# Performance work log

Hardware: AMD Instinct MI355X
Metric: run time of the kernel (lower is better)

## Reference

```python
import jax, jax.numpy as jnp
import numpy as np

B, L, D = 4, 2048, 512


def setup_inputs() -> dict:
    key = jax.random.key(0)
    ks = jax.random.split(key, 12)
    f32 = jnp.float32
    mk = lambda k, s: jax.random.normal(k, s, dtype=f32)
    # xavier-uniform-ish init scale for the linear weights
    w_qkv_lim = np.sqrt(6.0 / (6 * D + 6 * D)).astype(np.float32)
    w_out_lim = np.sqrt(6.0 / (2 * D + 2 * D)).astype(np.float32)
    return {
        "q_real": mk(ks[0], (B, L, D)),
        "q_imag": mk(ks[1], (B, L, D)),
        "k_real": mk(ks[2], (B, L, D)),
        "k_imag": mk(ks[3], (B, L, D)),
        "v_real": mk(ks[4], (B, L, D)),
        "v_imag": mk(ks[5], (B, L, D)),
        "pad_mask": jax.random.randint(ks[6], (B, L), 0, 2).astype(jnp.bool_),
        "W_qkv": jax.random.uniform(ks[7], (6 * D, 6 * D), f32, -w_qkv_lim, w_qkv_lim),
        "b_qkv": jnp.zeros((6 * D,), f32),
        "W_out": jax.random.uniform(ks[8], (2 * D, 2 * D), f32, -w_out_lim, w_out_lim),
        "b_out": jnp.zeros((2 * D,), f32),
    }


def reference(q_real, q_imag, k_real, k_imag, v_real, v_imag, pad_mask,
              W_qkv, b_qkv, W_out, b_out):
    b, l, d = q_real.shape
    # fused QKV projection over concatenated real/imag streams: [B, L, 6D]
    x = jnp.concatenate([q_real, q_imag, k_real, k_imag, v_real, v_imag], axis=-1)
    qkv = x @ W_qkv.T + b_qkv                      # torch Linear: x @ W^T + b
    qkv = qkv.reshape(b, l, 6, d)
    q_r, k_r = qkv[:, :, 0], qkv[:, :, 2]
    v_r, v_i = qkv[:, :, 4], qkv[:, :, 5]
    scale = jnp.asarray(d, jnp.float32) ** -0.5
    scores = jnp.einsum('bqd,bkd->bqk', q_r, k_r) * scale   # [B, L, L]
    scores = jnp.where(pad_mask[:, None, :], -jnp.inf, scores)
    attn = jax.nn.softmax(scores, axis=-1)         # dropout omitted (eval mode)
    out_real = jnp.einsum('bqk,bkd->bqd', attn, v_r)
    out_imag = jnp.einsum('bqk,bkd->bqd', attn, v_i)
    out = jnp.concatenate([out_real, out_imag], axis=-1) @ W_out.T + b_out
    return out[..., :d], out[..., d:]
```

## Files before the change

### kernel.cpp

```cpp
#include <hip/hip_runtime.h>
#include <cstdint>
#include <cstddef>

typedef unsigned short ushort;
typedef __attribute__((ext_vector_type(8))) short short8;
typedef __attribute__((ext_vector_type(16))) float f32x16;

__device__ __forceinline__ float bf2f(ushort u) {
  union { unsigned u; float f; } c; c.u = ((unsigned)u) << 16; return c.f;
}
__device__ __forceinline__ ushort f2bf(float f) {
  union { float f; unsigned u; } c; c.f = f;
  unsigned u = c.u;
  return (ushort)((u + 0x7fffu + ((u >> 16) & 1u)) >> 16);
}

#define G2L(g, l) __builtin_amdgcn_global_load_lds( \
    (const __attribute__((address_space(1))) void*)(g), \
    (__attribute__((address_space(3))) void*)(l), 16, 0, 0)

struct MArgs {
  const ushort* A; int lda; long asz;
  const ushort* B; int ldb; long bsz;
  void* C; int ldc; long csz;
  int K;
  const float* bias;
  float* C2;
};

template<int MODE, int BN>
__launch_bounds__(512, 2)
__global__ void mfma_gemm(MArgs g) {
  constexpr int BM = 256;
  constexpr int WN = BN / 64;
  constexpr int WM = 8 / WN;
  constexpr int WMSZ = BM / WM;
  constexpr int MF = WMSZ / 32;
  constexpr int NBG = BN / 64;
  constexpr int LPS = 4 + NBG;

  __shared__ __attribute__((aligned(16))) ushort As[2][BM * 64];
  __shared__ __attribute__((aligned(16))) ushort Bs[2][BN * 64];

  const int tid = threadIdx.x;
  const int lane = tid & 63;
  const int wave = tid >> 6;
  const int z = blockIdx.z;

  int bx = blockIdx.x, by = blockIdx.y;
  {
    const int gx = gridDim.x;
    const int nwg = gx * gridDim.y;
    int wg = by * gx + bx;
    wg = (wg & 7) * (nwg >> 3) + (wg >> 3);
    bx = wg % gx; by = wg / gx;
  }
  const long m0 = (long)by * BM;
  const long n0 = (long)bx * BN;
  const ushort* Ab = g.A + (long)z * g.asz;
  const ushort* Bb = g.B + (long)z * g.bsz;

  const int srow = tid >> 3;
  const long skel = (long)((((tid & 7) - srow) & 7) * 8);
  const ushort* ga[4];
  const ushort* gb[NBG];
#pragma unroll
  for (int q = 0; q < 4; ++q) ga[q] = Ab + (m0 + q * 64 + srow) * (long)g.lda + skel;
#pragma unroll
  for (int q = 0; q < NBG; ++q) gb[q] = Bb + (n0 + q * 64 + srow) * (long)g.ldb + skel;

  const int l31 = lane & 31, hb = lane >> 5;
  const int wmi = wave / WN, wni = wave % WN;
  int aoff[MF], arot[MF];
#pragma unroll
  for (int mf = 0; mf < MF; ++mf) {
    const int r = wmi * WMSZ + mf * 32 + l31;
    aoff[mf] = r * 64;
    arot[mf] = (r + hb) & 7;
  }
  int boff[2], brot[2];
#pragma unroll
  for (int nf = 0; nf < 2; ++nf) {
    const int r = wni * 64 + nf * 32 + l31;
    boff[nf] = r * 64;
    brot[nf] = (r + hb) & 7;
  }

  f32x16 acc[MF][2];
#pragma unroll
  for (int mf = 0; mf < MF; ++mf)
#pragma unroll
    for (int nf = 0; nf < 2; ++nf)
#pragma unroll
      for (int r = 0; r < 16; ++r) acc[mf][nf][r] = 0.f;

  auto STAGEF = [&](int buf, int t) {
    const long ko = (long)t * 64;
#pragma unroll
    for (int q = 0; q < 4; ++q) G2L(ga[q] + ko, &As[buf][q * 4096 + tid * 8]);
#pragma unroll
    for (int q = 0; q < NBG; ++q) G2L(gb[q] + ko, &Bs[buf][q * 4096 + tid * 8]);
  };

  STAGEF(0, 0);
  STAGEF(1, 1);

  const int nt = g.K >> 6;
  int cur = 0;
  for (int t = 0; t < nt; ++t) {
    if (t + 1 < nt) asm volatile("s_waitcnt vmcnt(%0)" :: "n"(LPS) : "memory");
    else            asm volatile("s_waitcnt vmcnt(0)" ::: "memory");
    __builtin_amdgcn_s_barrier();
    asm volatile("" ::: "memory");

    const ushort* as = &As[cur][0];
    const ushort* bs = &Bs[cur][0];
    __builtin_amdgcn_s_setprio(1);
#pragma unroll
    for (int h = 0; h < 4; ++h) {
      short8 av[MF], bv[2];
#pragma unroll
      for (int mf = 0; mf < MF; ++mf)
        av[mf] = *(const short8*)(as + aoff[mf] + (((2 * h + arot[mf]) & 7) << 3));
#pragma unroll
      for (int nf = 0; nf < 2; ++nf)
        bv[nf] = *(const short8*)(bs + boff[nf] + (((2 * h + brot[nf]) & 7) << 3));
#pragma unroll
      for (int mf = 0; mf < MF; ++mf)
#pragma unroll
        for (int nf = 0; nf < 2; ++nf)
          acc[mf][nf] = __builtin_amdgcn_mfma_f32_32x32x16_bf16(av[mf], bv[nf], acc[mf][nf], 0, 0, 0);
    }
    __builtin_amdgcn_s_setprio(0);

    asm volatile("s_waitcnt lgkmcnt(0)" ::: "memory");
    __builtin_amdgcn_s_barrier();
    asm volatile("" ::: "memory");
    if (t + 2 < nt) STAGEF(cur, t + 2);
    cur ^= 1;
  }

  const int cc = l31;
  const int rbase = 4 * hb;
  ushort* Cu = (ushort*)g.C + (long)z * g.csz;
  float* Cf = (float*)g.C;
#pragma unroll
  for (int mf = 0; mf < MF; ++mf) {
#pragma unroll
    for (int nf = 0; nf < 2; ++nf) {
      const long col = n0 + wni * 64 + nf * 32 + cc;
      float bsv = 0.f;
      if (MODE == 0 || MODE == 3) bsv = g.bias[col];
#pragma unroll
      for (int r = 0; r < 16; ++r) {
        const long row = m0 + wmi * WMSZ + mf * 32 + (r & 3) + 8 * (r >> 2) + rbase;
        float v = acc[mf][nf][r] + bsv;
        if (MODE == 3) {
          float* dst = (col < 512) ? (Cf + row * 512 + col) : (g.C2 + row * 512 + (col - 512));
          *dst = v;
        } else {
          Cu[row * (long)g.ldc + col] = f2bf(v);
        }
      }
    }
  }
}

__global__ void cvt_x6(const float* x0, const float* x1, const float* x2,
                       const float* x3, const float* x4, const float* x5, ushort* X) {
  const long m = blockIdx.y;
  const int c4 = (blockIdx.x * 256 + threadIdx.x) * 4;
  const int p = c4 >> 9, d = c4 & 511;
  const float* xp;
  switch (p) {
    case 0: xp = x0; break; case 1: xp = x1; break; case 2: xp = x2; break;
    case 3: xp = x3; break; case 4: xp = x4; break; default: xp = x5; break;
  }
  float4 v = *(const float4*)(xp + m * 512 + d);
  ushort4 o; o.x = f2bf(v.x); o.y = f2bf(v.y); o.z = f2bf(v.z); o.w = f2bf(v.w);
  *(ushort4*)(X + m * 3072 + c4) = o;
}

__device__ __forceinline__ int chunk_map(int c) { return (c == 0) ? 0 : (c == 1) ? 2 : (c == 2) ? 4 : 5; }

__global__ void cvt_w4(const float* W, ushort* Wq4) {
  const long r = blockIdx.y;
  const int c4 = (blockIdx.x * 256 + threadIdx.x) * 4;
  const long wr = (long)chunk_map((int)(r >> 9)) * 512 + (r & 511);
  float4 v = *(const float4*)(W + wr * 3072 + c4);
  ushort4 o; o.x = f2bf(v.x); o.y = f2bf(v.y); o.z = f2bf(v.z); o.w = f2bf(v.w);
  *(ushort4*)(Wq4 + r * 3072 + c4) = o;
}

__global__ void cvt_wout(const float* W, ushort* Wo) {
  const long r = blockIdx.y;
  const int c4 = threadIdx.x * 4;
  float4 v = *(const float4*)(W + r * 1024 + c4);
  ushort4 o; o.x = f2bf(v.x); o.y = f2bf(v.y); o.z = f2bf(v.z); o.w = f2bf(v.w);
  *(ushort4*)(Wo + r * 1024 + c4) = o;
}

__global__ void mk_bias4(const float* bqkv, float* b4) {
  const int n = blockIdx.x * 256 + threadIdx.x;
  b4[n] = bqkv[chunk_map(n >> 9) * 512 + (n & 511)];
}

__global__ void transpose_v(const ushort* QKV, ushort* Vt) {
  __shared__ ushort t[64][65];
  const int tid = threadIdx.x;
  const int k0 = blockIdx.x * 64, n0 = blockIdx.y * 64, b = blockIdx.z;
  const ushort* src = QKV + (long)b * 2048 * 2048 + 1024;
#pragma unroll
  for (int i = 0; i < 16; ++i) {
    int idx = i * 256 + tid; int r = idx >> 6, c = idx & 63;
    t[r][c] = src[(long)(k0 + r) * 2048 + (n0 + c)];
  }
  __syncthreads();
  ushort* dst = Vt + (long)b * 1024 * 2048;
#pragma unroll
  for (int i = 0; i < 16; ++i) {
    int idx = i * 256 + tid; int r = idx >> 6, c = idx & 63;
    dst[(long)(n0 + r) * 2048 + (k0 + c)] = t[c][r];
  }
}

__launch_bounds__(256)
__global__ void softmax_rows(ushort* S, const int* mask) {
  const int lane = threadIdx.x & 63;
  const int wave = threadIdx.x >> 6;
  const long row = (long)blockIdx.x * 4 + wave;
  const int* m = mask + (row >> 11) * 2048 + lane * 32;
  ushort* s = S + row * 2048 + lane * 32;
  const float scale = 0.04419417382415922f;

  short8 raw[4];
#pragma unroll
  for (int i = 0; i < 4; ++i) raw[i] = *(const short8*)(s + i * 8);
  int4 mi[8];
#pragma unroll
  for (int i = 0; i < 8; ++i) mi[i] = *(const int4*)(m + i * 4);

  float v[32];
  int mk[32];
#pragma unroll
  for (int i = 0; i < 8; ++i) {
    mk[i * 4 + 0] = mi[i].x; mk[i * 4 + 1] = mi[i].y;
    mk[i * 4 + 2] = mi[i].z; mk[i * 4 + 3] = mi[i].w;
  }
#pragma unroll
  for (int i = 0; i < 32; ++i) v[i] = bf2f((ushort)raw[i >> 3][i & 7]) * scale;

  float mx = -INFINITY;
#pragma unroll
  for (int i = 0; i < 32; ++i) if (!mk[i]) mx = fmaxf(mx, v[i]);
#pragma unroll
  for (int off = 32; off; off >>= 1) mx = fmaxf(mx, __shfl_xor(mx, off));

  float sum = 0.f;
#pragma unroll
  for (int i = 0; i < 32; ++i) {
    float e = mk[i] ? 0.f : __expf(v[i] - mx);
    v[i] = e;
    sum += e;
  }
#pragma unroll
  for (int off = 32; off; off >>= 1) sum += __shfl_xor(sum, off);

  float r = 1.f / sum;
  short8 out[4];
#pragma unroll
  for (int i = 0; i < 32; ++i) out[i >> 3][i & 7] = (short)f2bf(v[i] * r);
#pragma unroll
  for (int i = 0; i < 4; ++i) *(short8*)(s + i * 8) = out[i];
}

extern "C" void kernel_launch(void* const* d_in, const int* in_sizes, int n_in,
                              void* d_out, int out_size, void* d_ws, size_t ws_size,
                              hipStream_t stream) {
  const float* qr = (const float*)d_in[0];
  const float* qi = (const float*)d_in[1];
  const float* kr = (const float*)d_in[2];
  const float* ki = (const float*)d_in[3];
  const float* vr = (const float*)d_in[4];
  const float* vi = (const float*)d_in[5];
  const int* pm = (const int*)d_in[6];
  const float* Wqkv = (const float*)d_in[7];
  const float* bqkv = (const float*)d_in[8];
  const float* Wout = (const float*)d_in[9];
  const float* bout = (const float*)d_in[10];
  float* out = (float*)d_out;

  char* base = (char*)d_ws;
  ushort* QKV   = (ushort*)(base);
  ushort* Wq4   = (ushort*)(base + 33554432);
  ushort* Wo    = (ushort*)(base + 46137344);
  float*  b4    = (float*) (base + 48234496);
  char*   uni   = base + 48242688;
  ushort* Xbf   = (ushort*)(uni);
  ushort* Vt    = (ushort*)(uni);
  ushort* S     = (ushort*)(uni + 16777216);
  ushort* AO    = (ushort*)(uni + 50331648);

  cvt_x6<<<dim3(3, 8192), 256, 0, stream>>>(qr, qi, kr, ki, vr, vi, Xbf);
  cvt_w4<<<dim3(3, 2048), 256, 0, stream>>>(Wqkv, Wq4);
  cvt_wout<<<dim3(1, 1024), 256, 0, stream>>>(Wout, Wo);
  mk_bias4<<<8, 256, 0, stream>>>(bqkv, b4);

  {
    MArgs a{};
    a.A = Xbf; a.lda = 3072; a.asz = 0;
    a.B = Wq4; a.ldb = 3072; a.bsz = 0;
    a.C = QKV; a.ldc = 2048; a.csz = 0;
    a.K = 3072; a.bias = b4;
    mfma_gemm<0, 256><<<dim3(8, 32, 1), 512, 0, stream>>>(a);
  }

  transpose_v<<<dim3(32, 16, 4), 256, 0, stream>>>(QKV, Vt);

  {
    MArgs a{};
    a.A = QKV;        a.lda = 2048; a.asz = (long)2048 * 2048;
    a.B = QKV + 512;  a.ldb = 2048; a.bsz = (long)2048 * 2048;
    a.C = S;          a.ldc = 2048; a.csz = (long)2048 * 2048;
    a.K = 512;
    mfma_gemm<1, 256><<<dim3(8, 8, 4), 512, 0, stream>>>(a);
  }

  softmax_rows<<<2048, 256, 0, stream>>>(S, pm);

  {
    MArgs a{};
    a.A = S;  a.lda = 2048; a.asz = (long)2048 * 2048;
    a.B = Vt; a.ldb = 2048; a.bsz = (long)1024 * 2048;
    a.C = AO; a.ldc = 1024; a.csz = (long)2048 * 1024;
    a.K = 2048;
    mfma_gemm<2, 128><<<dim3(8, 8, 4), 512, 0, stream>>>(a);
  }

  {
    MArgs a{};
    a.A = AO; a.lda = 1024; a.asz = 0;
    a.B = Wo; a.ldb = 1024; a.bsz = 0;
    a.C = out; a.ldc = 512; a.csz = 0;
    a.C2 = out + (long)8192 * 512;
    a.K = 1024; a.bias = bout;
    mfma_gemm<3, 128><<<dim3(8, 32, 1), 512, 0, stream>>>(a);
  }
}
```

Measured before the change: 409.4 us.

## Restructure GEMM main loop to interleave LDS reads, MFMA and staged global loads

Splits the per-tile K loop into four phases that prefetch LDS fragments ahead of the MFMAs and issue the A and B global-to-LDS loads for tile t+2 between MFMA groups, with the barriers spread across the phases. The goal is to overlap LDS reads and global loads with matrix-core work instead of serialising them behind a single barrier. It also lowers the launch bounds to one block per SM, allowing more registers for the extra fragment buffers at the cost of occupancy.

```diff
diff --git a/kernel.cpp b/kernel.cpp
--- a/kernel.cpp
+++ b/kernel.cpp
@@ -18,6 +18,9 @@
 #define G2L(g, l) __builtin_amdgcn_global_load_lds( \
     (const __attribute__((address_space(1))) void*)(g), \
     (__attribute__((address_space(3))) void*)(l), 16, 0, 0)
+
+#define BARRIER() do { asm volatile("" ::: "memory"); __builtin_amdgcn_s_barrier(); asm volatile("" ::: "memory"); } while (0)
+#define LGKM0()   do { asm volatile("s_waitcnt lgkmcnt(0)" ::: "memory"); __builtin_amdgcn_sched_barrier(0); } while (0)
 
 struct MArgs {
   const ushort* A; int lda; long asz;
@@ -29,7 +32,7 @@
 };
 
 template<int MODE, int BN>
-__launch_bounds__(512, 2)
+__launch_bounds__(512, 1)
 __global__ void mfma_gemm(MArgs g) {
   constexpr int BM = 256;
   constexpr int WN = BN / 64;
@@ -94,50 +97,66 @@
 #pragma unroll
       for (int r = 0; r < 16; ++r) acc[mf][nf][r] = 0.f;
 
-  auto STAGEF = [&](int buf, int t) {
+  auto STAGE_A = [&](int buf, int t) {
     const long ko = (long)t * 64;
 #pragma unroll
     for (int q = 0; q < 4; ++q) G2L(ga[q] + ko, &As[buf][q * 4096 + tid * 8]);
+  };
+  auto STAGE_B = [&](int buf, int t) {
+    const long ko = (long)t * 64;
 #pragma unroll
     for (int q = 0; q < NBG; ++q) G2L(gb[q] + ko, &Bs[buf][q * 4096 + tid * 8]);
   };
 
-  STAGEF(0, 0);
-  STAGEF(1, 1);
+  STAGE_A(0, 0); STAGE_B(0, 0);
+  STAGE_A(1, 1); STAGE_B(1, 1);
+  asm volatile("s_waitcnt vmcnt(%0)" :: "n"(LPS) : "memory");
+  BARRIER();
 
   const int nt = g.K >> 6;
   int cur = 0;
   for (int t = 0; t < nt; ++t) {
-    if (t + 1 < nt) asm volatile("s_waitcnt vmcnt(%0)" :: "n"(LPS) : "memory");
-    else            asm volatile("s_waitcnt vmcnt(0)" ::: "memory");
-    __builtin_amdgcn_s_barrier();
-    asm volatile("" ::: "memory");
-
     const ushort* as = &As[cur][0];
     const ushort* bs = &Bs[cur][0];
-    __builtin_amdgcn_s_setprio(1);
-#pragma unroll
-    for (int h = 0; h < 4; ++h) {
-      short8 av[MF], bv[2];
-#pragma unroll
-      for (int mf = 0; mf < MF; ++mf)
-        av[mf] = *(const short8*)(as + aoff[mf] + (((2 * h + arot[mf]) & 7) << 3));
-#pragma unroll
-      for (int nf = 0; nf < 2; ++nf)
-        bv[nf] = *(const short8*)(bs + boff[nf] + (((2 * h + brot[nf]) & 7) << 3));
-#pragma unroll
-      for (int mf = 0; mf < MF; ++mf)
-#pragma unroll
-        for (int nf = 0; nf < 2; ++nf)
-          acc[mf][nf] = __builtin_amdgcn_mfma_f32_32x32x16_bf16(av[mf], bv[nf], acc[mf][nf], 0, 0, 0);
+    short8 av[4][MF], bv[4][2];
+
+#define READ_H(h) do { \
+  _Pragma("unroll") for (int mf = 0; mf < MF; ++mf) \
+    av[h][mf] = *(const short8*)(as + aoff[mf] + (((2 * (h) + arot[mf]) & 7) << 3)); \
+  _Pragma("unroll") for (int nf = 0; nf < 2; ++nf) \
+    bv[h][nf] = *(const short8*)(bs + boff[nf] + (((2 * (h) + brot[nf]) & 7) << 3)); \
+} while (0)
+#define MFMA_H(h) do { \
+  __builtin_amdgcn_s_setprio(1); \
+  _Pragma("unroll") for (int mf = 0; mf < MF; ++mf) \
+  _Pragma("unroll") for (int nf = 0; nf < 2; ++nf) \
+    acc[mf][nf] = __builtin_amdgcn_mfma_f32_32x32x16_bf16(av[h][mf], bv[h][nf], acc[mf][nf], 0, 0, 0); \
+  __builtin_amdgcn_s_setprio(0); \
+} while (0)
+
+    READ_H(0); READ_H(1);
+    MFMA_H(0);
+    BARRIER();
+
+    READ_H(2); READ_H(3);
+    MFMA_H(1);
+    LGKM0();
+    BARRIER();
+
+    if (t + 2 < nt) STAGE_A(cur, t + 2);
+    MFMA_H(2);
+    BARRIER();
+
+    if (t + 2 < nt) STAGE_B(cur, t + 2);
+    MFMA_H(3);
+    if (t + 1 < nt) {
+      if (t + 2 < nt) asm volatile("s_waitcnt vmcnt(%0)" :: "n"(LPS) : "memory");
+      else            asm volatile("s_waitcnt vmcnt(0)" ::: "memory");
+      BARRIER();
     }
-    __builtin_amdgcn_s_setprio(0);
-
-    asm volatile("s_waitcnt lgkmcnt(0)" ::: "memory");
-    __builtin_amdgcn_s_barrier();
-    asm volatile("" ::: "memory");
-    if (t + 2 < nt) STAGEF(cur, t + 2);
     cur ^= 1;
+#undef READ_H
+#undef MFMA_H
   }
 
   const int cc = l31;
```

After: 404.8 us. No clear change (-1.1%).

## Halve GEMM block to 256 threads with larger per-wave tiles and software-pipelined LDS reads

Applied to the files above, without the earlier changes.

Reworks the shared MFMA GEMM from 8 waves to 4 waves per 256x{256,128} tile, so each wave computes a bigger sub-tile (more accumulators per wave) and issues more global-to-LDS loads per stage. The inner K loop now double-buffers LDS fragment reads in registers, interleaving reads for the next k-step with MFMAs of the current one, and drops the setprio hints. The goal is more reuse per LDS read and better overlap of LDS latency with MFMA work, at the cost of much higher register pressure and one workgroup per CU, which may reduce latency hiding.

```diff
diff --git a/kernel.cpp b/kernel.cpp
--- a/kernel.cpp
+++ b/kernel.cpp
@@ -18,6 +18,9 @@
 #define G2L(g, l) __builtin_amdgcn_global_load_lds( \
     (const __attribute__((address_space(1))) void*)(g), \
     (__attribute__((address_space(3))) void*)(l), 16, 0, 0)
+
+#define BARRIER() do { asm volatile("" ::: "memory"); __builtin_amdgcn_s_barrier(); asm volatile("" ::: "memory"); } while (0)
+#define LGKM0()   do { asm volatile("s_waitcnt lgkmcnt(0)" ::: "memory"); __builtin_amdgcn_sched_barrier(0); } while (0)
 
 struct MArgs {
   const ushort* A; int lda; long asz;
@@ -29,15 +32,18 @@
 };
 
 template<int MODE, int BN>
-__launch_bounds__(512, 2)
+__launch_bounds__(256, 1)
 __global__ void mfma_gemm(MArgs g) {
   constexpr int BM = 256;
-  constexpr int WN = BN / 64;
-  constexpr int WM = 8 / WN;
+  constexpr int WN = (BN == 256) ? 2 : 1;
+  constexpr int WM = 4 / WN;
   constexpr int WMSZ = BM / WM;
+  constexpr int WNSZ = BN / WN;
   constexpr int MF = WMSZ / 32;
-  constexpr int NBG = BN / 64;
-  constexpr int LPS = 4 + NBG;
+  constexpr int NF = WNSZ / 32;
+  constexpr int NAG = BM / 32;
+  constexpr int NBG = BN / 32;
+  constexpr int LPS = NAG + NBG;
 
   __shared__ __attribute__((aligned(16))) ushort As[2][BM * 64];
   __shared__ __attribute__((aligned(16))) ushort Bs[2][BN * 64];
@@ -62,12 +68,10 @@
 
   const int srow = tid >> 3;
   const long skel = (long)((((tid & 7) - srow) & 7) * 8);
-  const ushort* ga[4];
-  const ushort* gb[NBG];
-#pragma unroll
-  for (int q = 0; q < 4; ++q) ga[q] = Ab + (m0 + q * 64 + srow) * (long)g.lda + skel;
-#pragma unroll
-  for (int q = 0; q < NBG; ++q) gb[q] = Bb + (n0 + q * 64 + srow) * (long)g.ldb + skel;
+  const ushort* ga0 = Ab + (m0 + srow) * (long)g.lda + skel;
+  const ushort* gb0 = Bb + (n0 + srow) * (long)g.ldb + skel;
+  const long astep = 32L * (long)g.lda;
+  const long bstep = 32L * (long)g.ldb;
 
   const int l31 = lane & 31, hb = lane >> 5;
   const int wmi = wave / WN, wni = wave % WN;
@@ -78,28 +82,32 @@
     aoff[mf] = r * 64;
     arot[mf] = (r + hb) & 7;
   }
-  int boff[2], brot[2];
-#pragma unroll
-  for (int nf = 0; nf < 2; ++nf) {
-    const int r = wni * 64 + nf * 32 + l31;
+  int boff[NF], brot[NF];
+#pragma unroll
+  for (int nf = 0; nf < NF; ++nf) {
+    const int r = wni * WNSZ + nf * 32 + l31;
     boff[nf] = r * 64;
     brot[nf] = (r + hb) & 7;
   }
 
-  f32x16 acc[MF][2];
+  f32x16 acc[MF][NF];
 #pragma unroll
   for (int mf = 0; mf < MF; ++mf)
 #pragma unroll
-    for (int nf = 0; nf < 2; ++nf)
+    for (int nf = 0; nf < NF; ++nf)
 #pragma unroll
       for (int r = 0; r < 16; ++r) acc[mf][nf][r] = 0.f;
 
   auto STAGEF = [&](int buf, int t) {
     const long ko = (long)t * 64;
-#pragma unroll
-    for (int q = 0; q < 4; ++q) G2L(ga[q] + ko, &As[buf][q * 4096 + tid * 8]);
-#pragma unroll
-    for (int q = 0; q < NBG; ++q) G2L(gb[q] + ko, &Bs[buf][q * 4096 + tid * 8]);
+    const ushort* p = ga0 + ko;
+    ushort* l = &As[buf][tid * 8];
+#pragma unroll
+    for (int q = 0; q < NAG; ++q) { G2L(p, l); p += astep; l += 2048; }
+    p = gb0 + ko;
+    l = &Bs[buf][tid * 8];
+#pragma unroll
+    for (int q = 0; q < NBG; ++q) { G2L(p, l); p += bstep; l += 2048; }
   };
 
   STAGEF(0, 0);
@@ -110,32 +118,37 @@
   for (int t = 0; t < nt; ++t) {
     if (t + 1 < nt) asm volatile("s_waitcnt vmcnt(%0)" :: "n"(LPS) : "memory");
     else            asm volatile("s_waitcnt vmcnt(0)" ::: "memory");
-    __builtin_amdgcn_s_barrier();
-    asm volatile("" ::: "memory");
+    BARRIER();
 
     const ushort* as = &As[cur][0];
     const ushort* bs = &Bs[cur][0];
-    __builtin_amdgcn_s_setprio(1);
-#pragma unroll
-    for (int h = 0; h < 4; ++h) {
-      short8 av[MF], bv[2];
-#pragma unroll
-      for (int mf = 0; mf < MF; ++mf)
-        av[mf] = *(const short8*)(as + aoff[mf] + (((2 * h + arot[mf]) & 7) << 3));
-#pragma unroll
-      for (int nf = 0; nf < 2; ++nf)
-        bv[nf] = *(const short8*)(bs + boff[nf] + (((2 * h + brot[nf]) & 7) << 3));
-#pragma unroll
-      for (int mf = 0; mf < MF; ++mf)
-#pragma unroll
-        for (int nf = 0; nf < 2; ++nf)
-          acc[mf][nf] = __builtin_amdgcn_mfma_f32_32x32x16_bf16(av[mf], bv[nf], acc[mf][nf], 0, 0, 0);
-    }
-    __builtin_amdgcn_s_setprio(0);
-
-    asm volatile("s_waitcnt lgkmcnt(0)" ::: "memory");
-    __builtin_amdgcn_s_barrier();
-    asm volatile("" ::: "memory");
+    short8 av[2][MF], bv[2][NF];
+
+#define READ_S(s, h) do { \
+  _Pragma("unroll") for (int mf = 0; mf < MF; ++mf) \
+    av[s][mf] = *(const short8*)(as + aoff[mf] + (((2 * (h) + arot[mf]) & 7) << 3)); \
+  _Pragma("unroll") for (int nf = 0; nf < NF; ++nf) \
+    bv[s][nf] = *(const short8*)(bs + boff[nf] + (((2 * (h) + brot[nf]) & 7) << 3)); \
+} while (0)
+#define MFMA_S(s) do { \
+  _Pragma("unroll") for (int mf = 0; mf < MF; ++mf) \
+  _Pragma("unroll") for (int nf = 0; nf < NF; ++nf) \
+    acc[mf][nf] = __builtin_amdgcn_mfma_f32_32x32x16_bf16(av[s][mf], bv[s][nf], acc[mf][nf], 0, 0, 0); \
+} while (0)
+
+    READ_S(0, 0);
+    READ_S(1, 1);
+    MFMA_S(0);
+    READ_S(0, 2);
+    MFMA_S(1);
+    READ_S(1, 3);
+    MFMA_S(0);
+    MFMA_S(1);
+#undef READ_S
+#undef MFMA_S
+
+    LGKM0();
+    BARRIER();
     if (t + 2 < nt) STAGEF(cur, t + 2);
     cur ^= 1;
   }
@@ -147,8 +160,8 @@
 #pragma unroll
   for (int mf = 0; mf < MF; ++mf) {
 #pragma unroll
-    for (int nf = 0; nf < 2; ++nf) {
-      const long col = n0 + wni * 64 + nf * 32 + cc;
+    for (int nf = 0; nf < NF; ++nf) {
+      const long col = n0 + wni * WNSZ + nf * 32 + cc;
       float bsv = 0.f;
       if (MODE == 0 || MODE == 3) bsv = g.bias[col];
 #pragma unroll
@@ -312,7 +325,7 @@
     a.B = Wq4; a.ldb = 3072; a.bsz = 0;
     a.C = QKV; a.ldc = 2048; a.csz = 0;
     a.K = 3072; a.bias = b4;
-    mfma_gemm<0, 256><<<dim3(8, 32, 1), 512, 0, stream>>>(a);
+    mfma_gemm<0, 256><<<dim3(8, 32, 1), 256, 0, stream>>>(a);
   }
 
   transpose_v<<<dim3(32, 16, 4), 256, 0, stream>>>(QKV, Vt);
@@ -323,7 +336,7 @@
     a.B = QKV + 512;  a.ldb = 2048; a.bsz = (long)2048 * 2048;
     a.C = S;          a.ldc = 2048; a.csz = (long)2048 * 2048;
     a.K = 512;
-    mfma_gemm<1, 256><<<dim3(8, 8, 4), 512, 0, stream>>>(a);
+    mfma_gemm<1, 256><<<dim3(8, 8, 4), 256, 0, stream>>>(a);
   }
 
   softmax_rows<<<2048, 256, 0, stream>>>(S, pm);
@@ -334,7 +347,7 @@
     a.B = Vt; a.ldb = 2048; a.bsz = (long)1024 * 2048;
     a.C = AO; a.ldc = 1024; a.csz = (long)2048 * 1024;
     a.K = 2048;
-    mfma_gemm<2, 128><<<dim3(8, 8, 4), 512, 0, stream>>>(a);
+    mfma_gemm<2, 128><<<dim3(8, 8, 4), 256, 0, stream>>>(a);
   }
 
   {
@@ -344,6 +357,6 @@
     a.C = out; a.ldc = 512; a.csz = 0;
     a.C2 = out + (long)8192 * 512;
     a.K = 1024; a.bias = bout;
-    mfma_gemm<3, 128><<<dim3(8, 32, 1), 512, 0, stream>>>(a);
-  }
-}
+    mfma_gemm<3, 128><<<dim3(8, 32, 1), 256, 0, stream>>>(a);
+  }
+}
```

New measurement: 436.9 us. +6.7%, slower.

## Software-pipeline LDS fragment reads with MFMA via inline ds_read and waitcnts

Applied to the files above, without the earlier changes.

Replaces compiler-scheduled LDS loads in the GEMM inner loop with explicit ds_read_b128 inline asm, double-buffered across k-substeps. Each substep's reads are issued before the previous substep's MFMAs, with partial lgkmcnt waits. The next global-to-LDS stage is issued before the final MFMA group so the load overlaps compute. This aims to hide LDS latency behind matrix ops, at the cost of more registers and fragile manual waitcnt accounting.

```diff
diff --git a/kernel.cpp b/kernel.cpp
--- a/kernel.cpp
+++ b/kernel.cpp
@@ -18,6 +18,13 @@
 #define G2L(g, l) __builtin_amdgcn_global_load_lds( \
     (const __attribute__((address_space(1))) void*)(g), \
     (__attribute__((address_space(3))) void*)(l), 16, 0, 0)
+
+#define BARRIER() do { asm volatile("" ::: "memory"); __builtin_amdgcn_s_barrier(); asm volatile("" ::: "memory"); } while (0)
+#define LGKMC(N) do { asm volatile("s_waitcnt lgkmcnt(%0)" :: "n"(N) : "memory"); __builtin_amdgcn_sched_barrier(0); } while (0)
+
+__device__ __forceinline__ unsigned ldsoff(const void* p) {
+  return (unsigned)(unsigned long long)(__attribute__((address_space(3))) const void*)p;
+}
 
 struct MArgs {
   const ushort* A; int lda; long asz;
@@ -38,6 +45,7 @@
   constexpr int MF = WMSZ / 32;
   constexpr int NBG = BN / 64;
   constexpr int LPS = 4 + NBG;
+  constexpr int RD = MF + 2;
 
   __shared__ __attribute__((aligned(16))) ushort As[2][BM * 64];
   __shared__ __attribute__((aligned(16))) ushort Bs[2][BN * 64];
@@ -71,18 +79,18 @@
 
   const int l31 = lane & 31, hb = lane >> 5;
   const int wmi = wave / WN, wni = wave % WN;
-  int aoff[MF], arot[MF];
+  unsigned aoffB[MF]; int arot[MF];
 #pragma unroll
   for (int mf = 0; mf < MF; ++mf) {
     const int r = wmi * WMSZ + mf * 32 + l31;
-    aoff[mf] = r * 64;
+    aoffB[mf] = (unsigned)(r * 128);
     arot[mf] = (r + hb) & 7;
   }
-  int boff[2], brot[2];
+  unsigned boffB[2]; int brot[2];
 #pragma unroll
   for (int nf = 0; nf < 2; ++nf) {
     const int r = wni * 64 + nf * 32 + l31;
-    boff[nf] = r * 64;
+    boffB[nf] = (unsigned)(r * 128);
     brot[nf] = (r + hb) & 7;
   }
 
@@ -106,38 +114,50 @@
   STAGEF(1, 1);
 
   const int nt = g.K >> 6;
-  int cur = 0;
   for (int t = 0; t < nt; ++t) {
+    const int cur = t & 1;
     if (t + 1 < nt) asm volatile("s_waitcnt vmcnt(%0)" :: "n"(LPS) : "memory");
     else            asm volatile("s_waitcnt vmcnt(0)" ::: "memory");
-    __builtin_amdgcn_s_barrier();
-    asm volatile("" ::: "memory");
-
-    const ushort* as = &As[cur][0];
-    const ushort* bs = &Bs[cur][0];
-    __builtin_amdgcn_s_setprio(1);
-#pragma unroll
-    for (int h = 0; h < 4; ++h) {
-      short8 av[MF], bv[2];
-#pragma unroll
-      for (int mf = 0; mf < MF; ++mf)
-        av[mf] = *(const short8*)(as + aoff[mf] + (((2 * h + arot[mf]) & 7) << 3));
-#pragma unroll
-      for (int nf = 0; nf < 2; ++nf)
-        bv[nf] = *(const short8*)(bs + boff[nf] + (((2 * h + brot[nf]) & 7) << 3));
-#pragma unroll
-      for (int mf = 0; mf < MF; ++mf)
-#pragma unroll
-        for (int nf = 0; nf < 2; ++nf)
-          acc[mf][nf] = __builtin_amdgcn_mfma_f32_32x32x16_bf16(av[mf], bv[nf], acc[mf][nf], 0, 0, 0);
-    }
-    __builtin_amdgcn_s_setprio(0);
-
-    asm volatile("s_waitcnt lgkmcnt(0)" ::: "memory");
-    __builtin_amdgcn_s_barrier();
-    asm volatile("" ::: "memory");
+    BARRIER();
+
+    const unsigned abase = ldsoff(&As[cur][0]);
+    const unsigned bbase = ldsoff(&Bs[cur][0]);
+    short8 av[2][MF], bv[2][2];
+
+#define ISSUE_H(s, h) do { \
+  _Pragma("unroll") for (int mf = 0; mf < MF; ++mf) { \
+    unsigned o = abase + aoffB[mf] + (unsigned)((((2 * (h) + arot[mf]) & 7) << 4)); \
+    asm volatile("ds_read_b128 %0, %1" : "=v"(av[s][mf]) : "v"(o)); \
+  } \
+  _Pragma("unroll") for (int nf = 0; nf < 2; ++nf) { \
+    unsigned o = bbase + boffB[nf] + (unsigned)((((2 * (h) + brot[nf]) & 7) << 4)); \
+    asm volatile("ds_read_b128 %0, %1" : "=v"(bv[s][nf]) : "v"(o)); \
+  } \
+} while (0)
+#define MFMA_S(s) do { \
+  __builtin_amdgcn_s_setprio(1); \
+  _Pragma("unroll") for (int mf = 0; mf < MF; ++mf) \
+  _Pragma("unroll") for (int nf = 0; nf < 2; ++nf) \
+    acc[mf][nf] = __builtin_amdgcn_mfma_f32_32x32x16_bf16(av[s][mf], bv[s][nf], acc[mf][nf], 0, 0, 0); \
+  __builtin_amdgcn_s_setprio(0); \
+} while (0)
+
+    ISSUE_H(0, 0);
+    ISSUE_H(1, 1);
+    LGKMC(RD);
+    MFMA_S(0);
+    ISSUE_H(0, 2);
+    LGKMC(RD);
+    MFMA_S(1);
+    ISSUE_H(1, 3);
+    LGKMC(RD);
+    MFMA_S(0);
+    LGKMC(0);
+    BARRIER();
     if (t + 2 < nt) STAGEF(cur, t + 2);
-    cur ^= 1;
+    MFMA_S(1);
+#undef ISSUE_H
+#undef MFMA_S
   }
 
   const int cc = l31;
```

Measured after the change: 391.8 us. 4.3% less time.
